# Kernel tuning notes

Hardware: AMD Instinct MI355X
Metric: run time of the kernel (lower is better)

Reference implementation:

```python
import jax, jax.numpy as jnp
import numpy as np

N_NODES = 100000


def gcn_conv(x, edge_index, W, b, num_nodes):
    # PyG GCNConv: h = x @ W; add self-loops; symmetric deg^-1/2 normalization;
    # out[dst] = sum_{src->dst} norm * h[src] + b
    h = x @ W
    loop = jnp.arange(num_nodes)
    src = jnp.concatenate([edge_index[0], loop])
    dst = jnp.concatenate([edge_index[1], loop])
    deg = jax.ops.segment_sum(jnp.ones_like(dst, dtype=h.dtype), dst, num_segments=num_nodes)
    dinv = jnp.where(deg > 0, jax.lax.rsqrt(deg), 0.0)
    norm = dinv[src] * dinv[dst]  # [E+N]
    msg = h[src] * norm[:, None]  # gather + scale
    out = jax.ops.segment_sum(msg, dst, num_segments=num_nodes)
    return out + b


def setup_inputs() -> dict:
    key = jax.random.key(0)
    k1, k2, k3, k4 = jax.random.split(key, 4)
    E = 3200000
    F_IN, HID, CLS = 512, 16, 7
    x = jax.random.normal(k1, (N_NODES, F_IN), dtype=jnp.float32)
    edge_index = jax.random.randint(k2, (2, E), 0, N_NODES, dtype=jnp.int64)
    W1 = jax.random.normal(k3, (F_IN, HID), dtype=jnp.float32) / np.sqrt(F_IN)
    b1 = jnp.zeros((HID,), dtype=jnp.float32)
    W2 = jax.random.normal(k4, (HID, CLS), dtype=jnp.float32) / np.sqrt(HID)
    b2 = jnp.zeros((CLS,), dtype=jnp.float32)
    return {"x": x, "edge_index": edge_index, "W1": W1, "b1": b1, "W2": W2, "b2": b2}


def reference(x, edge_index, W1, b1, W2, b2):
    h = gcn_conv(x, edge_index, W1, b1, N_NODES)
    h = jax.nn.relu(h)
    # dropout is identity in eval mode (p=0.5, training=False)
    out = gcn_conv(h, edge_index, W2, b2, N_NODES)
    return out
```

## Files before the change

### kernel.cpp

```cpp
#include <hip/hip_runtime.h>

#define N_NODES 100000
#define F_IN 512
#define HID 16
#define CLS 7

#define BK_SHIFT 8
#define BK_NODES 256
#define NBK ((N_NODES + BK_NODES - 1) / BK_NODES)
#define BK_CAP 9216

__global__ void detect_i64_kernel(const unsigned int* __restrict__ idx32,
                                  int* __restrict__ flag, int n_check) {
    __shared__ unsigned int s;
    if (threadIdx.x == 0) s = 0u;
    __syncthreads();
    unsigned int v = 0u;
    for (int i = threadIdx.x; i < n_check; i += blockDim.x)
        v |= idx32[2 * i + 1];
    atomicOr(&s, v);
    __syncthreads();
    if (threadIdx.x == 0) *flag = (s == 0u) ? 1 : 0;
}

__device__ __forceinline__ void get_edge(const void* eidx, long long E,
                                         long long e, int is64,
                                         int& s, int& d) {
    if (is64) {
        const long long* p = (const long long*)eidx;
        s = (int)p[e];
        d = (int)p[E + e];
    } else {
        const int* p = (const int*)eidx;
        s = p[e];
        d = p[E + e];
    }
}

#define SB_T 512
#define SB_TILE 4096

__global__ __launch_bounds__(SB_T) void scatter_bin_kernel(const void* __restrict__ eidx,
                                                           long long E,
                                                           const int* __restrict__ flag,
                                                           int* __restrict__ cursor,
                                                           unsigned int* __restrict__ binned) {
    __shared__ unsigned int stage[SB_TILE];
    __shared__ unsigned short stageb[SB_TILE];
    __shared__ int hist[NBK];
    __shared__ int excl[NBK];
    __shared__ int curs[NBK];
    __shared__ int gbase[NBK];
    __shared__ int scanv[SB_T];
    const int is64 = *flag;
    const int tid = threadIdx.x;
    const long long tileBeg = (long long)blockIdx.x * SB_TILE;
    long long rem = E - tileBeg;
    const int cnt = (int)(rem < SB_TILE ? rem : SB_TILE);

    for (int i = tid; i < NBK; i += SB_T) hist[i] = 0;
    __syncthreads();
    for (int i = tid; i < cnt; i += SB_T) {
        long long e = tileBeg + i;
        int d;
        if (is64) d = (int)((const long long*)eidx)[E + e];
        else      d = ((const int*)eidx)[E + e];
        atomicAdd(&hist[d >> BK_SHIFT], 1);
    }
    __syncthreads();
    scanv[tid] = (tid < NBK) ? hist[tid] : 0;
    __syncthreads();
    for (int off = 1; off < SB_T; off <<= 1) {
        int a = (tid >= off) ? scanv[tid - off] : 0;
        __syncthreads();
        scanv[tid] += a;
        __syncthreads();
    }
    if (tid < NBK) {
        int e = scanv[tid] - hist[tid];
        excl[tid] = e;
        curs[tid] = e;
    }
    __syncthreads();
    for (int i = tid; i < cnt; i += SB_T) {
        long long e = tileBeg + i;
        int s, d;
        get_edge(eidx, E, e, is64, s, d);
        int b = d >> BK_SHIFT;
        int pos = atomicAdd(&curs[b], 1);
        stage[pos] = ((unsigned int)(d & (BK_NODES - 1)) << 17) | (unsigned int)s;
        stageb[pos] = (unsigned short)b;
    }
    __syncthreads();
    if (tid < NBK) gbase[tid] = hist[tid]
        ? (tid * BK_CAP + atomicAdd(&cursor[tid], hist[tid])) : 0;
    __syncthreads();
    for (int i = tid; i < cnt; i += SB_T) {
        int b = stageb[i];
        int pos = gbase[b] + (i - excl[b]);
        if (pos < (b + 1) * BK_CAP)
            binned[pos] = stage[i];
    }
}

__global__ __launch_bounds__(256) void csr_build_kernel(const int* __restrict__ cursor,
                                                        unsigned int* __restrict__ binned,
                                                        float* __restrict__ dinv,
                                                        int* __restrict__ rowptr,
                                                        int* __restrict__ degA) {
    __shared__ unsigned int stage[BK_CAP];
    __shared__ int hist[BK_NODES];
    __shared__ int scanv[BK_NODES];
    __shared__ int curs[BK_NODES];
    const int tid = threadIdx.x;
    const int b = blockIdx.x;
    const int base = b * BK_CAP;
    int cnt = cursor[b];
    if (cnt > BK_CAP) cnt = BK_CAP;
    hist[tid] = 0;
    __syncthreads();
    for (int i = tid; i < cnt; i += 256)
        atomicAdd(&hist[binned[base + i] >> 17], 1);
    __syncthreads();
    scanv[tid] = hist[tid];
    __syncthreads();
    for (int off = 1; off < BK_NODES; off <<= 1) {
        int a = (tid >= off) ? scanv[tid - off] : 0;
        __syncthreads();
        scanv[tid] += a;
        __syncthreads();
    }
    {
        int e = scanv[tid] - hist[tid];
        curs[tid] = e;
        int g = b * BK_NODES + tid;
        if (g < N_NODES) {
            rowptr[g] = base + e;
            degA[g] = hist[tid];
            dinv[g] = rsqrtf((float)(hist[tid] + 1));
        }
    }
    __syncthreads();
    for (int i = tid; i < cnt; i += 256) {
        unsigned int v = binned[base + i];
        int pos = atomicAdd(&curs[(int)(v >> 17)], 1);
        stage[pos] = v & 0x1FFFFu;
    }
    __syncthreads();
    for (int i = tid; i < cnt; i += 256)
        binned[base + i] = stage[i];
}

#define G1_ROWS 64
#define G1_KC 64

__global__ __launch_bounds__(256) void gemm1_kernel(const float* __restrict__ x,
                                                    const float* __restrict__ W1,
                                                    const float* __restrict__ dinv,
                                                    float* __restrict__ h1s) {
    __shared__ float Ws[F_IN * HID];
    __shared__ float xs[G1_ROWS][G1_KC + 4];
    const int tid = threadIdx.x;
    const int rowBase = blockIdx.x * G1_ROWS;

#pragma unroll
    for (int it = 0; it < 8; it++) {
        int f = it * 256 + tid;
        ((float4*)Ws)[f] = ((const float4*)W1)[f];
    }

    const int r  = tid >> 2;
    const int j4 = tid & 3;
    float4 acc = make_float4(0.f, 0.f, 0.f, 0.f);

    for (int kc = 0; kc < F_IN; kc += G1_KC) {
        __syncthreads();
#pragma unroll
        for (int it = 0; it < 4; it++) {
            int f = it * 256 + tid;
            int row = f >> 4;
            int c4 = f & 15;
            int grow = rowBase + row;
            if (grow >= N_NODES) grow = N_NODES - 1;
            float4 v = ((const float4*)(x + (long long)grow * F_IN + kc))[c4];
            *((float4*)&xs[row][c4 * 4]) = v;
        }
        __syncthreads();
#pragma unroll
        for (int k = 0; k < G1_KC; k++) {
            float xv = xs[r][k];
            float4 wv = ((const float4*)(Ws + (kc + k) * HID))[j4];
            acc.x += xv * wv.x;
            acc.y += xv * wv.y;
            acc.z += xv * wv.z;
            acc.w += xv * wv.w;
        }
    }
    int grow = rowBase + r;
    if (grow < N_NODES) {
        float dn = dinv[grow];
        acc.x *= dn; acc.y *= dn; acc.z *= dn; acc.w *= dn;
        ((float4*)(h1s + (long long)grow * HID))[j4] = acc;
    }
}

#define A1_NODES 64

__global__ __launch_bounds__(256) void agg1_gemm2_kernel(const int* __restrict__ rowptr,
                                                         const int* __restrict__ degA,
                                                         const int* __restrict__ csr_src,
                                                         const float* __restrict__ h1s,
                                                         const float* __restrict__ dinv,
                                                         const float* __restrict__ b1,
                                                         const float* __restrict__ W2,
                                                         float* __restrict__ h2s) {
    __shared__ float W2s[HID][8];
    __shared__ float t_lds[A1_NODES][HID + 1];
    const int tid = threadIdx.x;
    if (tid < HID * 8) {
        int j = tid >> 3, c = tid & 7;
        W2s[j][c] = (c < CLS) ? W2[j * CLS + c] : 0.f;
    }
    const int ln = tid >> 2;
    const int j4 = tid & 3;
    const int n = blockIdx.x * A1_NODES + ln;
    float dn = 0.f;
    if (n < N_NODES) {
        const int beg = rowptr[n];
        const int end = beg + degA[n];
        const float4* h4 = (const float4*)h1s;
        float4 a0 = make_float4(0.f, 0.f, 0.f, 0.f);
        float4 a1 = make_float4(0.f, 0.f, 0.f, 0.f);
        int k = beg;
        for (; k + 4 <= end; k += 4) {
            int s0 = csr_src[k], s1 = csr_src[k + 1];
            int s2 = csr_src[k + 2], s3 = csr_src[k + 3];
            float4 v0 = h4[(long long)s0 * 4 + j4];
            float4 v1 = h4[(long long)s1 * 4 + j4];
            float4 v2 = h4[(long long)s2 * 4 + j4];
            float4 v3 = h4[(long long)s3 * 4 + j4];
            a0.x += v0.x; a0.y += v0.y; a0.z += v0.z; a0.w += v0.w;
            a1.x += v1.x; a1.y += v1.y; a1.z += v1.z; a1.w += v1.w;
            a0.x += v2.x; a0.y += v2.y; a0.z += v2.z; a0.w += v2.w;
            a1.x += v3.x; a1.y += v3.y; a1.z += v3.z; a1.w += v3.w;
        }
        for (; k < end; k++) {
            float4 v = h4[(long long)csr_src[k] * 4 + j4];
            a0.x += v.x; a0.y += v.y; a0.z += v.z; a0.w += v.w;
        }
        dn = dinv[n];
        float4 self = h4[(long long)n * 4 + j4];
        float4 bb = ((const float4*)b1)[j4];
        float* tp = &t_lds[ln][j4 * 4];
        tp[0] = fmaxf(bb.x + dn * (a0.x + a1.x + self.x), 0.f);
        tp[1] = fmaxf(bb.y + dn * (a0.y + a1.y + self.y), 0.f);
        tp[2] = fmaxf(bb.z + dn * (a0.z + a1.z + self.z), 0.f);
        tp[3] = fmaxf(bb.w + dn * (a0.w + a1.w + self.w), 0.f);
    }
    __syncthreads();
    if (n < N_NODES) {
        float b0 = 0.f, c1 = 0.f;
#pragma unroll
        for (int j = 0; j < HID; j++) {
            float v = t_lds[ln][j];
            b0 += v * W2s[j][2 * j4];
            c1 += v * W2s[j][2 * j4 + 1];
        }
        h2s[(long long)n * 8 + 2 * j4]     = dn * b0;
        h2s[(long long)n * 8 + 2 * j4 + 1] = dn * c1;
    }
}

#define A2_NODES 32

__global__ __launch_bounds__(256) void agg2_gather_kernel(const int* __restrict__ rowptr,
                                                          const int* __restrict__ degA,
                                                          const int* __restrict__ csr_src,
                                                          const float* __restrict__ h2s,
                                                          const float* __restrict__ dinv,
                                                          const float* __restrict__ b2,
                                                          float* __restrict__ out) {
    const int tid = threadIdx.x;
    const int ln = tid >> 3;
    const int c = tid & 7;
    const int n = blockIdx.x * A2_NODES + ln;
    if (n >= N_NODES) return;
    const int beg = rowptr[n];
    const int end = beg + degA[n];
    float a0 = 0.f, a1 = 0.f;
    int k = beg;
    for (; k + 4 <= end; k += 4) {
        int s0 = csr_src[k], s1 = csr_src[k + 1];
        int s2 = csr_src[k + 2], s3 = csr_src[k + 3];
        float v0 = h2s[(long long)s0 * 8 + c];
        float v1 = h2s[(long long)s1 * 8 + c];
        float v2 = h2s[(long long)s2 * 8 + c];
        float v3 = h2s[(long long)s3 * 8 + c];
        a0 += v0 + v2;
        a1 += v1 + v3;
    }
    for (; k < end; k++)
        a0 += h2s[(long long)csr_src[k] * 8 + c];
    if (c < CLS)
        out[(long long)n * CLS + c] =
            b2[c] + dinv[n] * (h2s[(long long)n * 8 + c] + a0 + a1);
}

extern "C" void kernel_launch(void* const* d_in, const int* in_sizes, int n_in,
                              void* d_out, int out_size, void* d_ws, size_t ws_size,
                              hipStream_t stream) {
    const float* x    = (const float*)d_in[0];
    const void*  eidx = d_in[1];
    const float* W1   = (const float*)d_in[2];
    const float* b1   = (const float*)d_in[3];
    const float* W2   = (const float*)d_in[4];
    const float* b2   = (const float*)d_in[5];
    float* out = (float*)d_out;
    const long long E = (long long)in_sizes[1] / 2;

    char* ws = (char*)d_ws;
    size_t off = 0;
    auto alloc = [&](size_t bytes) -> void* {
        void* p = ws + off;
        off = (off + bytes + 255) & ~(size_t)255;
        return p;
    };
    int*          flag   = (int*)alloc(4);
    int*          cursor = (int*)alloc((size_t)NBK * 4);
    unsigned int* binned = (unsigned int*)alloc((size_t)NBK * BK_CAP * 4);
    int*          rowptr = (int*)alloc((size_t)N_NODES * 4);
    int*          degA   = (int*)alloc((size_t)N_NODES * 4);
    float*        dinv   = (float*)alloc((size_t)N_NODES * 4);
    float*        h1s    = (float*)alloc((size_t)N_NODES * HID * 4);
    float*        h2s    = (float*)alloc((size_t)N_NODES * 8 * 4);
    (void)ws_size;

    hipMemsetAsync(cursor, 0, (size_t)NBK * 4, stream);

    detect_i64_kernel<<<1, 256, 0, stream>>>((const unsigned int*)eidx, flag,
                                             (int)(E < 4096 ? E : 4096));

    scatter_bin_kernel<<<(int)((E + SB_TILE - 1) / SB_TILE), SB_T, 0, stream>>>(
        eidx, E, flag, cursor, binned);

    csr_build_kernel<<<NBK, 256, 0, stream>>>(cursor, binned, dinv, rowptr, degA);

    gemm1_kernel<<<(N_NODES + G1_ROWS - 1) / G1_ROWS, 256, 0, stream>>>(x, W1, dinv, h1s);

    const int* csr_src = (const int*)binned;
    agg1_gemm2_kernel<<<(N_NODES + A1_NODES - 1) / A1_NODES, 256, 0, stream>>>(
        rowptr, degA, csr_src, h1s, dinv, b1, W2, h2s);

    agg2_gather_kernel<<<(N_NODES + A2_NODES - 1) / A2_NODES, 256, 0, stream>>>(
        rowptr, degA, csr_src, h2s, dinv, b2, out);
}
```

Before: 445.3 us.

## Restructure binning, CSR build, GEMM tiling and gather kernels with vector loads

Scatter-binning now holds edges in registers and claims output slots with shared-memory atomics instead of a block scan and LDS staging. It also reads edge pairs with vector loads and processes larger tiles. The CSR build uses 512 threads, loads each bucket once into LDS with uint4 reads, and scatters directly to global memory. GEMM1 computes two rows per thread with float4 LDS reads. Both aggregation kernels use int4 index loads, unroll by 8 with four accumulators, and layer 2 uses float4 gathers with two threads per node. The cursor memset is folded into the detect kernel. Together these aim to cut memory traffic, launch overhead and latency stalls. Edges within a bucket lose their deterministic order, so float summation order varies between runs.

```diff
diff --git a/kernel.cpp b/kernel.cpp
--- a/kernel.cpp
+++ b/kernel.cpp
@@ -10,8 +10,13 @@
 #define NBK ((N_NODES + BK_NODES - 1) / BK_NODES)
 #define BK_CAP 9216
 
+#define ADD4(a, v) { (a).x += (v).x; (a).y += (v).y; (a).z += (v).z; (a).w += (v).w; }
+#define FMA4(acc, sc, wv) { (acc).x += (sc)*(wv).x; (acc).y += (sc)*(wv).y; (acc).z += (sc)*(wv).z; (acc).w += (sc)*(wv).w; }
+
 __global__ void detect_i64_kernel(const unsigned int* __restrict__ idx32,
-                                  int* __restrict__ flag, int n_check) {
+                                  int* __restrict__ flag, int n_check,
+                                  int* __restrict__ cursor) {
+    for (int i = threadIdx.x; i < NBK; i += blockDim.x) cursor[i] = 0;
     __shared__ unsigned int s;
     if (threadIdx.x == 0) s = 0u;
     __syncthreads();
@@ -23,87 +28,83 @@
     if (threadIdx.x == 0) *flag = (s == 0u) ? 1 : 0;
 }
 
-__device__ __forceinline__ void get_edge(const void* eidx, long long E,
-                                         long long e, int is64,
-                                         int& s, int& d) {
-    if (is64) {
-        const long long* p = (const long long*)eidx;
-        s = (int)p[e];
-        d = (int)p[E + e];
-    } else {
-        const int* p = (const int*)eidx;
-        s = p[e];
-        d = p[E + e];
-    }
-}
-
 #define SB_T 512
-#define SB_TILE 4096
+#define SB_TILE 8192
+#define SB_EPT (SB_TILE / SB_T)
 
 __global__ __launch_bounds__(SB_T) void scatter_bin_kernel(const void* __restrict__ eidx,
                                                            long long E,
                                                            const int* __restrict__ flag,
                                                            int* __restrict__ cursor,
                                                            unsigned int* __restrict__ binned) {
-    __shared__ unsigned int stage[SB_TILE];
-    __shared__ unsigned short stageb[SB_TILE];
     __shared__ int hist[NBK];
-    __shared__ int excl[NBK];
-    __shared__ int curs[NBK];
-    __shared__ int gbase[NBK];
-    __shared__ int scanv[SB_T];
+    __shared__ int gcur[NBK];
     const int is64 = *flag;
     const int tid = threadIdx.x;
     const long long tileBeg = (long long)blockIdx.x * SB_TILE;
-    long long rem = E - tileBeg;
-    const int cnt = (int)(rem < SB_TILE ? rem : SB_TILE);
+    const bool evE = ((E & 1LL) == 0LL);
 
     for (int i = tid; i < NBK; i += SB_T) hist[i] = 0;
     __syncthreads();
-    for (int i = tid; i < cnt; i += SB_T) {
-        long long e = tileBeg + i;
-        int d;
-        if (is64) d = (int)((const long long*)eidx)[E + e];
-        else      d = ((const int*)eidx)[E + e];
-        atomicAdd(&hist[d >> BK_SHIFT], 1);
-    }
-    __syncthreads();
-    scanv[tid] = (tid < NBK) ? hist[tid] : 0;
-    __syncthreads();
-    for (int off = 1; off < SB_T; off <<= 1) {
-        int a = (tid >= off) ? scanv[tid - off] : 0;
-        __syncthreads();
-        scanv[tid] += a;
-        __syncthreads();
-    }
-    if (tid < NBK) {
-        int e = scanv[tid] - hist[tid];
-        excl[tid] = e;
-        curs[tid] = e;
-    }
-    __syncthreads();
-    for (int i = tid; i < cnt; i += SB_T) {
-        long long e = tileBeg + i;
-        int s, d;
-        get_edge(eidx, E, e, is64, s, d);
-        int b = d >> BK_SHIFT;
-        int pos = atomicAdd(&curs[b], 1);
-        stage[pos] = ((unsigned int)(d & (BK_NODES - 1)) << 17) | (unsigned int)s;
-        stageb[pos] = (unsigned short)b;
-    }
-    __syncthreads();
-    if (tid < NBK) gbase[tid] = hist[tid]
-        ? (tid * BK_CAP + atomicAdd(&cursor[tid], hist[tid])) : 0;
-    __syncthreads();
-    for (int i = tid; i < cnt; i += SB_T) {
-        int b = stageb[i];
-        int pos = gbase[b] + (i - excl[b]);
-        if (pos < (b + 1) * BK_CAP)
-            binned[pos] = stage[i];
-    }
-}
-
-__global__ __launch_bounds__(256) void csr_build_kernel(const int* __restrict__ cursor,
+
+    unsigned int vv[SB_EPT];
+    int bb[SB_EPT];
+
+#pragma unroll
+    for (int j = 0; j < SB_EPT / 2; j++) {
+        long long e = tileBeg + (long long)j * (2 * SB_T) + 2 * tid;
+        int s0 = 0, d0 = 0, s1 = 0, d1 = 0;
+        const bool ok0 = e < E, ok1 = (e + 1) < E;
+        if (is64) {
+            const long long* p = (const long long*)eidx;
+            if (ok1 && evE) {
+                longlong2 sp = *(const longlong2*)(p + e);
+                longlong2 dp = *(const longlong2*)(p + E + e);
+                s0 = (int)sp.x; s1 = (int)sp.y; d0 = (int)dp.x; d1 = (int)dp.y;
+            } else {
+                if (ok0) { s0 = (int)p[e];     d0 = (int)p[E + e]; }
+                if (ok1) { s1 = (int)p[e + 1]; d1 = (int)p[E + e + 1]; }
+            }
+        } else {
+            const int* p = (const int*)eidx;
+            if (ok1 && evE) {
+                int2 sp = *(const int2*)(p + e);
+                int2 dp = *(const int2*)(p + E + e);
+                s0 = sp.x; s1 = sp.y; d0 = dp.x; d1 = dp.y;
+            } else {
+                if (ok0) { s0 = p[e];     d0 = p[E + e]; }
+                if (ok1) { s1 = p[e + 1]; d1 = p[E + e + 1]; }
+            }
+        }
+        if (ok0) {
+            int b = d0 >> BK_SHIFT;
+            bb[2 * j] = b;
+            vv[2 * j] = ((unsigned int)(d0 & (BK_NODES - 1)) << 17) | (unsigned int)s0;
+            atomicAdd(&hist[b], 1);
+        } else bb[2 * j] = -1;
+        if (ok1) {
+            int b = d1 >> BK_SHIFT;
+            bb[2 * j + 1] = b;
+            vv[2 * j + 1] = ((unsigned int)(d1 & (BK_NODES - 1)) << 17) | (unsigned int)s1;
+            atomicAdd(&hist[b], 1);
+        } else bb[2 * j + 1] = -1;
+    }
+    __syncthreads();
+    for (int i = tid; i < NBK; i += SB_T)
+        gcur[i] = hist[i] ? (i * BK_CAP + atomicAdd(&cursor[i], hist[i])) : 0;
+    __syncthreads();
+#pragma unroll
+    for (int j = 0; j < SB_EPT; j++) {
+        int b = bb[j];
+        if (b >= 0) {
+            int pos = atomicAdd(&gcur[b], 1);
+            if (pos < (b + 1) * BK_CAP)
+                binned[pos] = vv[j];
+        }
+    }
+}
+
+__global__ __launch_bounds__(512) void csr_build_kernel(const int* __restrict__ cursor,
                                                         unsigned int* __restrict__ binned,
                                                         float* __restrict__ dinv,
                                                         int* __restrict__ rowptr,
@@ -117,20 +118,33 @@
     const int base = b * BK_CAP;
     int cnt = cursor[b];
     if (cnt > BK_CAP) cnt = BK_CAP;
-    hist[tid] = 0;
-    __syncthreads();
-    for (int i = tid; i < cnt; i += 256)
-        atomicAdd(&hist[binned[base + i] >> 17], 1);
-    __syncthreads();
-    scanv[tid] = hist[tid];
+    if (tid < BK_NODES) hist[tid] = 0;
+    __syncthreads();
+    const int cnt4 = cnt >> 2;
+    for (int i = tid; i < cnt4; i += 512) {
+        uint4 u = ((const uint4*)(binned + base))[i];
+        ((uint4*)stage)[i] = u;
+        atomicAdd(&hist[u.x >> 17], 1);
+        atomicAdd(&hist[u.y >> 17], 1);
+        atomicAdd(&hist[u.z >> 17], 1);
+        atomicAdd(&hist[u.w >> 17], 1);
+    }
+    for (int i = (cnt4 << 2) + tid; i < cnt; i += 512) {
+        unsigned int u = binned[base + i];
+        stage[i] = u;
+        atomicAdd(&hist[u >> 17], 1);
+    }
+    __syncthreads();
+    if (tid < BK_NODES) scanv[tid] = hist[tid];
     __syncthreads();
     for (int off = 1; off < BK_NODES; off <<= 1) {
-        int a = (tid >= off) ? scanv[tid - off] : 0;
+        int a = 0;
+        if (tid < BK_NODES && tid >= off) a = scanv[tid - off];
         __syncthreads();
-        scanv[tid] += a;
+        if (tid < BK_NODES) scanv[tid] += a;
         __syncthreads();
     }
-    {
+    if (tid < BK_NODES) {
         int e = scanv[tid] - hist[tid];
         curs[tid] = e;
         int g = b * BK_NODES + tid;
@@ -141,25 +155,30 @@
         }
     }
     __syncthreads();
-    for (int i = tid; i < cnt; i += 256) {
-        unsigned int v = binned[base + i];
-        int pos = atomicAdd(&curs[(int)(v >> 17)], 1);
-        stage[pos] = v & 0x1FFFFu;
-    }
-    __syncthreads();
-    for (int i = tid; i < cnt; i += 256)
-        binned[base + i] = stage[i];
-}
-
-#define G1_ROWS 64
-#define G1_KC 64
+    for (int i = tid; i < cnt4; i += 512) {
+        uint4 u = ((const uint4*)stage)[i];
+        int p0 = atomicAdd(&curs[(int)(u.x >> 17)], 1); binned[base + p0] = u.x & 0x1FFFFu;
+        int p1 = atomicAdd(&curs[(int)(u.y >> 17)], 1); binned[base + p1] = u.y & 0x1FFFFu;
+        int p2 = atomicAdd(&curs[(int)(u.z >> 17)], 1); binned[base + p2] = u.z & 0x1FFFFu;
+        int p3 = atomicAdd(&curs[(int)(u.w >> 17)], 1); binned[base + p3] = u.w & 0x1FFFFu;
+    }
+    for (int i = (cnt4 << 2) + tid; i < cnt; i += 512) {
+        unsigned int u = stage[i];
+        int p = atomicAdd(&curs[(int)(u >> 17)], 1);
+        binned[base + p] = u & 0x1FFFFu;
+    }
+}
+
+#define G1_ROWS 128
+#define G1_KC 32
+#define G1_LDX (G1_KC + 4)
 
 __global__ __launch_bounds__(256) void gemm1_kernel(const float* __restrict__ x,
                                                     const float* __restrict__ W1,
                                                     const float* __restrict__ dinv,
                                                     float* __restrict__ h1s) {
     __shared__ float Ws[F_IN * HID];
-    __shared__ float xs[G1_ROWS][G1_KC + 4];
+    __shared__ float xs[G1_ROWS][G1_LDX];
     const int tid = threadIdx.x;
     const int rowBase = blockIdx.x * G1_ROWS;
 
@@ -171,36 +190,48 @@
 
     const int r  = tid >> 2;
     const int j4 = tid & 3;
-    float4 acc = make_float4(0.f, 0.f, 0.f, 0.f);
+    float4 accA = make_float4(0.f, 0.f, 0.f, 0.f);
+    float4 accB = make_float4(0.f, 0.f, 0.f, 0.f);
+    const float4* Wf4 = (const float4*)Ws;
 
     for (int kc = 0; kc < F_IN; kc += G1_KC) {
         __syncthreads();
 #pragma unroll
         for (int it = 0; it < 4; it++) {
             int f = it * 256 + tid;
-            int row = f >> 4;
-            int c4 = f & 15;
+            int row = f >> 3;
+            int c4 = f & 7;
             int grow = rowBase + row;
             if (grow >= N_NODES) grow = N_NODES - 1;
-            float4 v = ((const float4*)(x + (long long)grow * F_IN + kc))[c4];
-            *((float4*)&xs[row][c4 * 4]) = v;
+            *((float4*)&xs[row][c4 * 4]) = ((const float4*)(x + (long long)grow * F_IN + kc))[c4];
         }
         __syncthreads();
 #pragma unroll
-        for (int k = 0; k < G1_KC; k++) {
-            float xv = xs[r][k];
-            float4 wv = ((const float4*)(Ws + (kc + k) * HID))[j4];
-            acc.x += xv * wv.x;
-            acc.y += xv * wv.y;
-            acc.z += xv * wv.z;
-            acc.w += xv * wv.w;
-        }
-    }
-    int grow = rowBase + r;
-    if (grow < N_NODES) {
-        float dn = dinv[grow];
-        acc.x *= dn; acc.y *= dn; acc.z *= dn; acc.w *= dn;
-        ((float4*)(h1s + (long long)grow * HID))[j4] = acc;
+        for (int k4 = 0; k4 < G1_KC / 4; k4++) {
+            float4 xa = *(const float4*)&xs[r][k4 * 4];
+            float4 xb = *(const float4*)&xs[r + 64][k4 * 4];
+            int kb = (kc + k4 * 4) * 4 + j4;
+            float4 w0 = Wf4[kb];
+            float4 w1 = Wf4[kb + 4];
+            float4 w2 = Wf4[kb + 8];
+            float4 w3 = Wf4[kb + 12];
+            FMA4(accA, xa.x, w0); FMA4(accA, xa.y, w1);
+            FMA4(accA, xa.z, w2); FMA4(accA, xa.w, w3);
+            FMA4(accB, xb.x, w0); FMA4(accB, xb.y, w1);
+            FMA4(accB, xb.z, w2); FMA4(accB, xb.w, w3);
+        }
+    }
+    int g0 = rowBase + r;
+    if (g0 < N_NODES) {
+        float dn = dinv[g0];
+        ((float4*)(h1s + (long long)g0 * HID))[j4] =
+            make_float4(accA.x * dn, accA.y * dn, accA.z * dn, accA.w * dn);
+    }
+    int g1 = rowBase + 64 + r;
+    if (g1 < N_NODES) {
+        float dn = dinv[g1];
+        ((float4*)(h1s + (long long)g1 * HID))[j4] =
+            make_float4(accB.x * dn, accB.y * dn, accB.z * dn, accB.w * dn);
     }
 }
 
@@ -231,31 +262,48 @@
         const float4* h4 = (const float4*)h1s;
         float4 a0 = make_float4(0.f, 0.f, 0.f, 0.f);
         float4 a1 = make_float4(0.f, 0.f, 0.f, 0.f);
+        float4 a2 = make_float4(0.f, 0.f, 0.f, 0.f);
+        float4 a3 = make_float4(0.f, 0.f, 0.f, 0.f);
         int k = beg;
-        for (; k + 4 <= end; k += 4) {
-            int s0 = csr_src[k], s1 = csr_src[k + 1];
-            int s2 = csr_src[k + 2], s3 = csr_src[k + 3];
-            float4 v0 = h4[(long long)s0 * 4 + j4];
-            float4 v1 = h4[(long long)s1 * 4 + j4];
-            float4 v2 = h4[(long long)s2 * 4 + j4];
-            float4 v3 = h4[(long long)s3 * 4 + j4];
-            a0.x += v0.x; a0.y += v0.y; a0.z += v0.z; a0.w += v0.w;
-            a1.x += v1.x; a1.y += v1.y; a1.z += v1.z; a1.w += v1.w;
-            a0.x += v2.x; a0.y += v2.y; a0.z += v2.z; a0.w += v2.w;
-            a1.x += v3.x; a1.y += v3.y; a1.z += v3.z; a1.w += v3.w;
+        for (; k < end && (k & 3); k++) {
+            float4 v = h4[(long long)csr_src[k] * 4 + j4];
+            ADD4(a0, v);
+        }
+        for (; k + 8 <= end; k += 8) {
+            int4 s0 = *(const int4*)(csr_src + k);
+            int4 s1 = *(const int4*)(csr_src + k + 4);
+            float4 v0 = h4[(long long)s0.x * 4 + j4];
+            float4 v1 = h4[(long long)s0.y * 4 + j4];
+            float4 v2 = h4[(long long)s0.z * 4 + j4];
+            float4 v3 = h4[(long long)s0.w * 4 + j4];
+            float4 v4 = h4[(long long)s1.x * 4 + j4];
+            float4 v5 = h4[(long long)s1.y * 4 + j4];
+            float4 v6 = h4[(long long)s1.z * 4 + j4];
+            float4 v7 = h4[(long long)s1.w * 4 + j4];
+            ADD4(a0, v0); ADD4(a1, v1); ADD4(a2, v2); ADD4(a3, v3);
+            ADD4(a0, v4); ADD4(a1, v5); ADD4(a2, v6); ADD4(a3, v7);
+        }
+        if (k + 4 <= end) {
+            int4 s0 = *(const int4*)(csr_src + k);
+            float4 v0 = h4[(long long)s0.x * 4 + j4];
+            float4 v1 = h4[(long long)s0.y * 4 + j4];
+            float4 v2 = h4[(long long)s0.z * 4 + j4];
+            float4 v3 = h4[(long long)s0.w * 4 + j4];
+            ADD4(a0, v0); ADD4(a1, v1); ADD4(a2, v2); ADD4(a3, v3);
+            k += 4;
         }
         for (; k < end; k++) {
             float4 v = h4[(long long)csr_src[k] * 4 + j4];
-            a0.x += v.x; a0.y += v.y; a0.z += v.z; a0.w += v.w;
+            ADD4(a0, v);
         }
         dn = dinv[n];
         float4 self = h4[(long long)n * 4 + j4];
         float4 bb = ((const float4*)b1)[j4];
         float* tp = &t_lds[ln][j4 * 4];
-        tp[0] = fmaxf(bb.x + dn * (a0.x + a1.x + self.x), 0.f);
-        tp[1] = fmaxf(bb.y + dn * (a0.y + a1.y + self.y), 0.f);
-        tp[2] = fmaxf(bb.z + dn * (a0.z + a1.z + self.z), 0.f);
-        tp[3] = fmaxf(bb.w + dn * (a0.w + a1.w + self.w), 0.f);
+        tp[0] = fmaxf(bb.x + dn * (a0.x + a1.x + a2.x + a3.x + self.x), 0.f);
+        tp[1] = fmaxf(bb.y + dn * (a0.y + a1.y + a2.y + a3.y + self.y), 0.f);
+        tp[2] = fmaxf(bb.z + dn * (a0.z + a1.z + a2.z + a3.z + self.z), 0.f);
+        tp[3] = fmaxf(bb.w + dn * (a0.w + a1.w + a2.w + a3.w + self.w), 0.f);
     }
     __syncthreads();
     if (n < N_NODES) {
@@ -271,7 +319,7 @@
     }
 }
 
-#define A2_NODES 32
+#define A2_NODES 128
 
 __global__ __launch_bounds__(256) void agg2_gather_kernel(const int* __restrict__ rowptr,
                                                           const int* __restrict__ degA,
@@ -281,29 +329,66 @@
                                                           const float* __restrict__ b2,
                                                           float* __restrict__ out) {
     const int tid = threadIdx.x;
-    const int ln = tid >> 3;
-    const int c = tid & 7;
+    const int ln = tid >> 1;
+    const int half = tid & 1;
     const int n = blockIdx.x * A2_NODES + ln;
     if (n >= N_NODES) return;
     const int beg = rowptr[n];
     const int end = beg + degA[n];
-    float a0 = 0.f, a1 = 0.f;
+    const float4* h4 = (const float4*)h2s;
+    float4 a0 = make_float4(0.f, 0.f, 0.f, 0.f);
+    float4 a1 = make_float4(0.f, 0.f, 0.f, 0.f);
+    float4 a2 = make_float4(0.f, 0.f, 0.f, 0.f);
+    float4 a3 = make_float4(0.f, 0.f, 0.f, 0.f);
     int k = beg;
-    for (; k + 4 <= end; k += 4) {
-        int s0 = csr_src[k], s1 = csr_src[k + 1];
-        int s2 = csr_src[k + 2], s3 = csr_src[k + 3];
-        float v0 = h2s[(long long)s0 * 8 + c];
-        float v1 = h2s[(long long)s1 * 8 + c];
-        float v2 = h2s[(long long)s2 * 8 + c];
-        float v3 = h2s[(long long)s3 * 8 + c];
-        a0 += v0 + v2;
-        a1 += v1 + v3;
-    }
-    for (; k < end; k++)
-        a0 += h2s[(long long)csr_src[k] * 8 + c];
-    if (c < CLS)
-        out[(long long)n * CLS + c] =
-            b2[c] + dinv[n] * (h2s[(long long)n * 8 + c] + a0 + a1);
+    for (; k < end && (k & 3); k++) {
+        float4 v = h4[(long long)csr_src[k] * 2 + half];
+        ADD4(a0, v);
+    }
+    for (; k + 8 <= end; k += 8) {
+        int4 s0 = *(const int4*)(csr_src + k);
+        int4 s1 = *(const int4*)(csr_src + k + 4);
+        float4 v0 = h4[(long long)s0.x * 2 + half];
+        float4 v1 = h4[(long long)s0.y * 2 + half];
+        float4 v2 = h4[(long long)s0.z * 2 + half];
+        float4 v3 = h4[(long long)s0.w * 2 + half];
+        float4 v4 = h4[(long long)s1.x * 2 + half];
+        float4 v5 = h4[(long long)s1.y * 2 + half];
+        float4 v6 = h4[(long long)s1.z * 2 + half];
+        float4 v7 = h4[(long long)s1.w * 2 + half];
+        ADD4(a0, v0); ADD4(a1, v1); ADD4(a2, v2); ADD4(a3, v3);
+        ADD4(a0, v4); ADD4(a1, v5); ADD4(a2, v6); ADD4(a3, v7);
+    }
+    if (k + 4 <= end) {
+        int4 s0 = *(const int4*)(csr_src + k);
+        float4 v0 = h4[(long long)s0.x * 2 + half];
+        float4 v1 = h4[(long long)s0.y * 2 + half];
+        float4 v2 = h4[(long long)s0.z * 2 + half];
+        float4 v3 = h4[(long long)s0.w * 2 + half];
+        ADD4(a0, v0); ADD4(a1, v1); ADD4(a2, v2); ADD4(a3, v3);
+        k += 4;
+    }
+    for (; k < end; k++) {
+        float4 v = h4[(long long)csr_src[k] * 2 + half];
+        ADD4(a0, v);
+    }
+    float dn = dinv[n];
+    float4 self = h4[(long long)n * 2 + half];
+    float tx = self.x + a0.x + a1.x + a2.x + a3.x;
+    float ty = self.y + a0.y + a1.y + a2.y + a3.y;
+    float tz = self.z + a0.z + a1.z + a2.z + a3.z;
+    float tw = self.w + a0.w + a1.w + a2.w + a3.w;
+    long long ob = (long long)n * CLS;
+    if (half == 0) {
+        out[ob + 0] = b2[0] + dn * tx;
+        out[ob + 1] = b2[1] + dn * ty;
+        out[ob + 2] = b2[2] + dn * tz;
+        out[ob + 3] = b2[3] + dn * tw;
+    } else {
+        out[ob + 4] = b2[4] + dn * tx;
+        out[ob + 5] = b2[5] + dn * ty;
+        out[ob + 6] = b2[6] + dn * tz;
+    }
 }
 
 extern "C" void kernel_launch(void* const* d_in, const int* in_sizes, int n_in,
@@ -335,15 +420,13 @@
     float*        h2s    = (float*)alloc((size_t)N_NODES * 8 * 4);
     (void)ws_size;
 
-    hipMemsetAsync(cursor, 0, (size_t)NBK * 4, stream);
-
     detect_i64_kernel<<<1, 256, 0, stream>>>((const unsigned int*)eidx, flag,
-                                             (int)(E < 4096 ? E : 4096));
+                                             (int)(E < 4096 ? E : 4096), cursor);
 
     scatter_bin_kernel<<<(int)((E + SB_TILE - 1) / SB_TILE), SB_T, 0, stream>>>(
         eidx, E, flag, cursor, binned);
 
-    csr_build_kernel<<<NBK, 256, 0, stream>>>(cursor, binned, dinv, rowptr, degA);
+    csr_build_kernel<<<NBK, 512, 0, stream>>>(cursor, binned, dinv, rowptr, degA);
 
     gemm1_kernel<<<(N_NODES + G1_ROWS - 1) / G1_ROWS, 256, 0, stream>>>(x, W1, dinv, h1s);
 
```

Result: no change. 450.3 us (+1.1%).
